# Optimization experiments

Measured on AMD Instinct MI355X. Metric: run time of the kernel, lower is better.

Reference implementation:

```python
import jax, jax.numpy as jnp
import numpy as np

B, L, D = 8, 4096, 1024
H, BS = 16, 4          # num_heads, block_size
d = D // H             # per-head dim


def setup_inputs() -> dict:
    ks = jax.random.split(jax.random.key(0), 4)
    x = jax.random.normal(ks[0], (B, L, D), dtype=jnp.float32)
    W_qkv = jax.random.normal(ks[1], (D, 3 * D), dtype=jnp.float32) * 0.02
    b_qkv = jnp.zeros((3 * D,), dtype=jnp.float32)
    W_proj = jax.random.normal(ks[2], (D, D), dtype=jnp.float32) * 0.02
    b_proj = jnp.zeros((D,), dtype=jnp.float32)
    return {"x": x, "W_qkv": W_qkv, "b_qkv": b_qkv,
            "W_proj": W_proj, "b_proj": b_proj}


def reference(x, W_qkv, b_qkv, W_proj, b_proj):
    scale = d ** -0.5
    n = L // BS  # number of blocks (L divisible by BS -> no padding/mask path)
    # qkv projection: (B, L, 3D); per-head layout [q(d) | k(d) | v(d)]
    qkv = x @ W_qkv + b_qkv
    qkv = qkv.reshape(B, L, H, 3 * d)
    q, k, v = qkv[..., :d], qkv[..., d:2 * d], qkv[..., 2 * d:]
    # (B, L, H, d) -> (B, H, n, BS, d)
    def to_blocks(t):
        return t.transpose(0, 2, 1, 3).reshape(B, H, n, BS, d)
    q, k, v = to_blocks(q), to_blocks(k), to_blocks(v)
    # block-local attention: tiny (BS x BS) score matrices per block
    attn = jnp.einsum('bhnid,bhnjd->bhnij', q, k) * scale
    attn = jax.nn.softmax(attn, axis=-1)
    o = jnp.einsum('bhnij,bhnjd->bhnid', attn, v)
    # (B, H, n, BS, d) -> (B, L, D)
    o = o.reshape(B, H, L, d).transpose(0, 2, 1, 3).reshape(B, L, D)
    return o @ W_proj + b_proj
```

## Files before the change

kernel.cpp:

```cpp
#include <hip/hip_runtime.h>
#include <hip/hip_bf16.h>

typedef __bf16 bf16_t;
typedef __bf16 bf16x4 __attribute__((ext_vector_type(4)));
typedef __bf16 bf16x8 __attribute__((ext_vector_type(8)));
typedef float  f32x4  __attribute__((ext_vector_type(4)));

#define D1   1024
#define D3   3072
#define NTOK 32768
#define NH   16

__device__ __forceinline__ void gl16(const void* g, void* l) {
  __builtin_amdgcn_global_load_lds(
      (__attribute__((address_space(1))) void*)(void*)g,
      (__attribute__((address_space(3))) void*)l, 16, 0, 0);
}

__global__ __launch_bounds__(256) void k0_convert(
    const float* __restrict__ x, bf16_t* __restrict__ xb)
{
  const size_t i = ((size_t)blockIdx.x * 256 + threadIdx.x) * 8;
  const float4 v0 = *reinterpret_cast<const float4*>(&x[i]);
  const float4 v1 = *reinterpret_cast<const float4*>(&x[i + 4]);
  bf16x8 o;
  o[0] = (bf16_t)v0.x; o[1] = (bf16_t)v0.y; o[2] = (bf16_t)v0.z; o[3] = (bf16_t)v0.w;
  o[4] = (bf16_t)v1.x; o[5] = (bf16_t)v1.y; o[6] = (bf16_t)v1.z; o[7] = (bf16_t)v1.w;
  *reinterpret_cast<bf16x8*>(&xb[i]) = o;
}

__global__ __launch_bounds__(256) void k0_transpose(
    const float* __restrict__ W, bf16_t* __restrict__ Wt, int K, int N)
{
  __shared__ float tile[32][33];
  const int k0 = blockIdx.x * 32, n0 = blockIdx.y * 32;
  const int tx = threadIdx.x & 31, ty = threadIdx.x >> 5;
#pragma unroll
  for (int i = 0; i < 4; ++i)
    tile[ty + i * 8][tx] = W[(size_t)(k0 + ty + i * 8) * N + n0 + tx];
  __syncthreads();
#pragma unroll
  for (int i = 0; i < 4; ++i)
    Wt[(size_t)(n0 + ty + i * 8) * K + k0 + tx] = (bf16_t)tile[tx][ty + i * 8];
}

__global__ __launch_bounds__(512, 4) void k1_qkv_attn(
    const bf16_t* __restrict__ xb, const bf16_t* __restrict__ Wt,
    const float* __restrict__ bqkv, bf16_t* __restrict__ o)
{
  __shared__ __align__(16) unsigned char smem[53248];
  bf16_t (*Ss)[200] = reinterpret_cast<bf16_t(*)[200]>(smem);
  float*  Ps        = reinterpret_cast<float*>(smem + 128 * 200 * 2);

  const int tid  = threadIdx.x;
  const int wv   = tid >> 6, lane = tid & 63;
  const int lrow = lane & 15, lkg = lane >> 4;
  const int wr   = wv >> 2, wc = wv & 3;
  const int m0   = blockIdx.x * 128;
  const int h    = blockIdx.y;

  const int lr = lane >> 3;
  const int lc = (lane & 7) * 8;
  const bf16_t* aS0 = xb + (size_t)(m0 + (wv * 2 + 0) * 8 + lr) * D1 + lc;
  const bf16_t* aS1 = xb + (size_t)(m0 + (wv * 2 + 1) * 8 + lr) * D1 + lc;
  char* aD0 = (char*)smem + (wv * 2 + 0) * 1024;
  char* aD1 = (char*)smem + (wv * 2 + 1) * 1024;
  const bf16_t* bS0 = Wt + (size_t)(h * 192 + (wv * 3 + 0) * 8 + lr) * D1 + lc;
  const bf16_t* bS1 = Wt + (size_t)(h * 192 + (wv * 3 + 1) * 8 + lr) * D1 + lc;
  const bf16_t* bS2 = Wt + (size_t)(h * 192 + (wv * 3 + 2) * 8 + lr) * D1 + lc;
  char* bD0 = (char*)smem + 16384 + (wv * 3 + 0) * 1024;
  char* bD1 = (char*)smem + 16384 + (wv * 3 + 1) * 1024;
  char* bD2 = (char*)smem + 16384 + (wv * 3 + 2) * 1024;

  f32x4 acc[4][3];
#pragma unroll
  for (int i = 0; i < 4; ++i)
#pragma unroll
    for (int j = 0; j < 3; ++j) {
      f32x4 z = {0.f, 0.f, 0.f, 0.f};
      acc[i][j] = z;
    }

  const char* As = (const char*)smem;
  const char* Bs = (const char*)smem + 16384;

  for (int k0 = 0; k0 < D1; k0 += 64) {
    gl16(aS0 + k0, aD0);
    gl16(aS1 + k0, aD1);
    gl16(bS0 + k0, bD0);
    gl16(bS1 + k0, bD1);
    gl16(bS2 + k0, bD2);
    __syncthreads();
#pragma unroll
    for (int kk = 0; kk < 2; ++kk) {
      bf16x8 a[4];
#pragma unroll
      for (int rf = 0; rf < 4; ++rf)
        a[rf] = *reinterpret_cast<const bf16x8*>(
            As + (wr * 64 + rf * 16 + lrow) * 128 + kk * 64 + lkg * 16);
#pragma unroll
      for (int cf = 0; cf < 3; ++cf) {
        const bf16x8 b = *reinterpret_cast<const bf16x8*>(
            Bs + (wc * 48 + cf * 16 + lrow) * 128 + kk * 64 + lkg * 16);
#pragma unroll
        for (int rf = 0; rf < 4; ++rf)
          acc[rf][cf] = __builtin_amdgcn_mfma_f32_16x16x32_bf16(
              a[rf], b, acc[rf][cf], 0, 0, 0);
      }
    }
    __syncthreads();
  }

#pragma unroll
  for (int cf = 0; cf < 3; ++cf) {
    const int col = wc * 48 + cf * 16 + lrow;
    const float bias = bqkv[h * 192 + col];
#pragma unroll
    for (int rf = 0; rf < 4; ++rf) {
      const int row = wr * 64 + rf * 16 + lkg * 4;
#pragma unroll
      for (int r = 0; r < 4; ++r)
        Ss[row + r][col] = (bf16_t)(acc[rf][cf][r] + bias);
    }
  }
  __syncthreads();

  {
    const int blk = tid >> 4, qi = (tid >> 2) & 3, kj = tid & 3;
    float s = 0.f;
#pragma unroll
    for (int c8 = 0; c8 < 8; ++c8) {
      const bf16x8 qv = *reinterpret_cast<const bf16x8*>(&Ss[blk * 4 + qi][c8 * 8]);
      const bf16x8 kv = *reinterpret_cast<const bf16x8*>(&Ss[blk * 4 + kj][64 + c8 * 8]);
#pragma unroll
      for (int u = 0; u < 8; ++u) s += (float)qv[u] * (float)kv[u];
    }
    s *= 0.125f;
    float mx = fmaxf(s, __shfl_xor(s, 1));
    mx = fmaxf(mx, __shfl_xor(mx, 2));
    const float e = __expf(s - mx);
    float sum = e + __shfl_xor(e, 1);
    sum += __shfl_xor(sum, 2);
    Ps[tid] = e / sum;
  }
  __syncthreads();

  {
    const int row = tid >> 2;
    const int blk = row >> 2, qi = row & 3;
    const int c0 = (tid & 3) * 16;
    const float p0 = Ps[blk * 16 + qi * 4 + 0];
    const float p1 = Ps[blk * 16 + qi * 4 + 1];
    const float p2 = Ps[blk * 16 + qi * 4 + 2];
    const float p3 = Ps[blk * 16 + qi * 4 + 3];
    bf16x8 outv[2];
#pragma unroll
    for (int hf = 0; hf < 2; ++hf) {
      const bf16x8 v0 = *reinterpret_cast<const bf16x8*>(&Ss[blk * 4 + 0][128 + c0 + hf * 8]);
      const bf16x8 v1 = *reinterpret_cast<const bf16x8*>(&Ss[blk * 4 + 1][128 + c0 + hf * 8]);
      const bf16x8 v2 = *reinterpret_cast<const bf16x8*>(&Ss[blk * 4 + 2][128 + c0 + hf * 8]);
      const bf16x8 v3 = *reinterpret_cast<const bf16x8*>(&Ss[blk * 4 + 3][128 + c0 + hf * 8]);
#pragma unroll
      for (int u = 0; u < 8; ++u)
        outv[hf][u] = (bf16_t)(p0 * (float)v0[u] + p1 * (float)v1[u] +
                               p2 * (float)v2[u] + p3 * (float)v3[u]);
    }
    bf16_t* dst = &o[(size_t)(m0 + row) * D1 + h * 64 + c0];
    *reinterpret_cast<bf16x8*>(dst)     = outv[0];
    *reinterpret_cast<bf16x8*>(dst + 8) = outv[1];
  }
}

__global__ __launch_bounds__(256, 2) void k2_proj(
    const bf16_t* __restrict__ o, const bf16_t* __restrict__ Wpt,
    const float* __restrict__ bp, float* __restrict__ out)
{
  __shared__ __align__(16) unsigned char smem2[32768];

  const int tid  = threadIdx.x;
  const int wv   = tid >> 6, lane = tid & 63;
  const int lrow = lane & 15, lkg = lane >> 4;
  const int wr   = wv >> 1, wc = wv & 1;
  const int m0   = blockIdx.x * 128, n0 = blockIdx.y * 128;

  const int lr = lane >> 3;
  const int lc = (lane & 7) * 8;
  const bf16_t* aSrc[4];
  const bf16_t* bSrc[4];
  char *aDst[4], *bDst[4];
#pragma unroll
  for (int i = 0; i < 4; ++i) {
    const int ch = wv * 4 + i;
    aSrc[i] = o   + (size_t)(m0 + ch * 8 + lr) * D1 + lc;
    bSrc[i] = Wpt + (size_t)(n0 + ch * 8 + lr) * D1 + lc;
    aDst[i] = (char*)smem2 + ch * 1024;
    bDst[i] = (char*)smem2 + 16384 + ch * 1024;
  }

  f32x4 acc[4][4];
#pragma unroll
  for (int i = 0; i < 4; ++i)
#pragma unroll
    for (int j = 0; j < 4; ++j) {
      f32x4 z = {0.f, 0.f, 0.f, 0.f};
      acc[i][j] = z;
    }

  const char* As = (const char*)smem2;
  const char* Bs = (const char*)smem2 + 16384;

  for (int k0 = 0; k0 < D1; k0 += 64) {
#pragma unroll
    for (int i = 0; i < 4; ++i) {
      gl16(aSrc[i] + k0, aDst[i]);
      gl16(bSrc[i] + k0, bDst[i]);
    }
    __syncthreads();
#pragma unroll
    for (int kk = 0; kk < 2; ++kk) {
      bf16x8 a[4], b[4];
#pragma unroll
      for (int rf = 0; rf < 4; ++rf)
        a[rf] = *reinterpret_cast<const bf16x8*>(
            As + (wr * 64 + rf * 16 + lrow) * 128 + kk * 64 + lkg * 16);
#pragma unroll
      for (int cf = 0; cf < 4; ++cf)
        b[cf] = *reinterpret_cast<const bf16x8*>(
            Bs + (wc * 64 + cf * 16 + lrow) * 128 + kk * 64 + lkg * 16);
#pragma unroll
      for (int rf = 0; rf < 4; ++rf)
#pragma unroll
        for (int cf = 0; cf < 4; ++cf)
          acc[rf][cf] = __builtin_amdgcn_mfma_f32_16x16x32_bf16(
              a[rf], b[cf], acc[rf][cf], 0, 0, 0);
    }
    __syncthreads();
  }

#pragma unroll
  for (int cf = 0; cf < 4; ++cf) {
    const int col = n0 + wc * 64 + cf * 16 + lrow;
    const float bias = bp[col];
#pragma unroll
    for (int rf = 0; rf < 4; ++rf) {
      const size_t row = (size_t)m0 + wr * 64 + rf * 16 + lkg * 4;
#pragma unroll
      for (int r = 0; r < 4; ++r)
        out[(row + r) * D1 + col] = acc[rf][cf][r] + bias;
    }
  }
}

extern "C" void kernel_launch(void* const* d_in, const int* in_sizes, int n_in,
                              void* d_out, int out_size, void* d_ws, size_t ws_size,
                              hipStream_t stream)
{
  const float* x    = (const float*)d_in[0];
  const float* Wqkv = (const float*)d_in[1];
  const float* bqkv = (const float*)d_in[2];
  const float* Wp   = (const float*)d_in[3];
  const float* bp   = (const float*)d_in[4];
  float* out        = (float*)d_out;

  bf16_t* xb   = (bf16_t*)d_ws;
  bf16_t* o_ws = xb   + (size_t)NTOK * D1;
  bf16_t* wtq  = o_ws + (size_t)NTOK * D1;
  bf16_t* wtp  = wtq  + (size_t)D3 * D1;

  k0_convert<<<NTOK * D1 / (256 * 8), 256, 0, stream>>>(x, xb);
  k0_transpose<<<dim3(D1 / 32, D3 / 32), 256, 0, stream>>>(Wqkv, wtq, D1, D3);
  k0_transpose<<<dim3(D1 / 32, D1 / 32), 256, 0, stream>>>(Wp,   wtp, D1, D1);
  k1_qkv_attn<<<dim3(NTOK / 128, NH), 512, 0, stream>>>(xb, wtq, bqkv, o_ws);
  k2_proj<<<dim3(NTOK / 128, D1 / 128), 256, 0, stream>>>(o_ws, wtp, bp, out);
}
```

Before: 603.8 us.

## Swizzle LDS layout, remap block order per XCD, raise occupancy bounds

Applies an XOR swizzle to the LDS tile layout in both GEMM kernels. Global-load source columns are permuted and the MFMA fragment reads use the matching XOR offset, which should remove LDS bank conflicts on the 128-byte-stride rows. Launches both kernels on a 1D grid and remaps block IDs so that blocks sharing an XCD (blockIdx mod 8) work on neighbouring tiles, improving L2 reuse of A rows and weights. Raises the launch_bounds min-blocks hint, which may force register spills.

```diff
diff --git a/kernel.cpp b/kernel.cpp
--- a/kernel.cpp
+++ b/kernel.cpp
@@ -2,7 +2,6 @@
 #include <hip/hip_bf16.h>
 
 typedef __bf16 bf16_t;
-typedef __bf16 bf16x4 __attribute__((ext_vector_type(4)));
 typedef __bf16 bf16x8 __attribute__((ext_vector_type(8)));
 typedef float  f32x4  __attribute__((ext_vector_type(4)));
 
@@ -44,7 +43,7 @@
     Wt[(size_t)(n0 + ty + i * 8) * K + k0 + tx] = (bf16_t)tile[tx][ty + i * 8];
 }
 
-__global__ __launch_bounds__(512, 4) void k1_qkv_attn(
+__global__ __launch_bounds__(512, 6) void k1_qkv_attn(
     const bf16_t* __restrict__ xb, const bf16_t* __restrict__ Wt,
     const float* __restrict__ bqkv, bf16_t* __restrict__ o)
 {
@@ -56,18 +55,20 @@
   const int wv   = tid >> 6, lane = tid & 63;
   const int lrow = lane & 15, lkg = lane >> 4;
   const int wr   = wv >> 2, wc = wv & 3;
-  const int m0   = blockIdx.x * 128;
-  const int h    = blockIdx.y;
-
-  const int lr = lane >> 3;
-  const int lc = (lane & 7) * 8;
-  const bf16_t* aS0 = xb + (size_t)(m0 + (wv * 2 + 0) * 8 + lr) * D1 + lc;
-  const bf16_t* aS1 = xb + (size_t)(m0 + (wv * 2 + 1) * 8 + lr) * D1 + lc;
+
+  const int logical = (blockIdx.x & 7) * 512 + (blockIdx.x >> 3);
+  const int h  = logical & 15;
+  const int m0 = (logical >> 4) * 128;
+
+  const int lr  = lane >> 3;
+  const int lcs = ((lane & 7) ^ lr) * 8;
+  const bf16_t* aS0 = xb + (size_t)(m0 + (wv * 2 + 0) * 8 + lr) * D1 + lcs;
+  const bf16_t* aS1 = xb + (size_t)(m0 + (wv * 2 + 1) * 8 + lr) * D1 + lcs;
   char* aD0 = (char*)smem + (wv * 2 + 0) * 1024;
   char* aD1 = (char*)smem + (wv * 2 + 1) * 1024;
-  const bf16_t* bS0 = Wt + (size_t)(h * 192 + (wv * 3 + 0) * 8 + lr) * D1 + lc;
-  const bf16_t* bS1 = Wt + (size_t)(h * 192 + (wv * 3 + 1) * 8 + lr) * D1 + lc;
-  const bf16_t* bS2 = Wt + (size_t)(h * 192 + (wv * 3 + 2) * 8 + lr) * D1 + lc;
+  const bf16_t* bS0 = Wt + (size_t)(h * 192 + (wv * 3 + 0) * 8 + lr) * D1 + lcs;
+  const bf16_t* bS1 = Wt + (size_t)(h * 192 + (wv * 3 + 1) * 8 + lr) * D1 + lcs;
+  const bf16_t* bS2 = Wt + (size_t)(h * 192 + (wv * 3 + 2) * 8 + lr) * D1 + lcs;
   char* bD0 = (char*)smem + 16384 + (wv * 3 + 0) * 1024;
   char* bD1 = (char*)smem + 16384 + (wv * 3 + 1) * 1024;
   char* bD2 = (char*)smem + 16384 + (wv * 3 + 2) * 1024;
@@ -83,6 +84,7 @@
 
   const char* As = (const char*)smem;
   const char* Bs = (const char*)smem + 16384;
+  const int sw = (lrow & 7) << 4;
 
   for (int k0 = 0; k0 < D1; k0 += 64) {
     gl16(aS0 + k0, aD0);
@@ -93,15 +95,16 @@
     __syncthreads();
 #pragma unroll
     for (int kk = 0; kk < 2; ++kk) {
+      const int koff = (kk * 64 + lkg * 16) ^ sw;
       bf16x8 a[4];
 #pragma unroll
       for (int rf = 0; rf < 4; ++rf)
         a[rf] = *reinterpret_cast<const bf16x8*>(
-            As + (wr * 64 + rf * 16 + lrow) * 128 + kk * 64 + lkg * 16);
+            As + (wr * 64 + rf * 16 + lrow) * 128 + koff);
 #pragma unroll
       for (int cf = 0; cf < 3; ++cf) {
         const bf16x8 b = *reinterpret_cast<const bf16x8*>(
-            Bs + (wc * 48 + cf * 16 + lrow) * 128 + kk * 64 + lkg * 16);
+            Bs + (wc * 48 + cf * 16 + lrow) * 128 + koff);
 #pragma unroll
         for (int rf = 0; rf < 4; ++rf)
           acc[rf][cf] = __builtin_amdgcn_mfma_f32_16x16x32_bf16(
@@ -171,7 +174,7 @@
   }
 }
 
-__global__ __launch_bounds__(256, 2) void k2_proj(
+__global__ __launch_bounds__(256, 3) void k2_proj(
     const bf16_t* __restrict__ o, const bf16_t* __restrict__ Wpt,
     const float* __restrict__ bp, float* __restrict__ out)
 {
@@ -181,18 +184,21 @@
   const int wv   = tid >> 6, lane = tid & 63;
   const int lrow = lane & 15, lkg = lane >> 4;
   const int wr   = wv >> 1, wc = wv & 1;
-  const int m0   = blockIdx.x * 128, n0 = blockIdx.y * 128;
-
-  const int lr = lane >> 3;
-  const int lc = (lane & 7) * 8;
+
+  const int logical = (blockIdx.x & 7) * 256 + (blockIdx.x >> 3);
+  const int n0 = (logical & 7) * 128;
+  const int m0 = (logical >> 3) * 128;
+
+  const int lr  = lane >> 3;
+  const int lcs = ((lane & 7) ^ lr) * 8;
   const bf16_t* aSrc[4];
   const bf16_t* bSrc[4];
   char *aDst[4], *bDst[4];
 #pragma unroll
   for (int i = 0; i < 4; ++i) {
     const int ch = wv * 4 + i;
-    aSrc[i] = o   + (size_t)(m0 + ch * 8 + lr) * D1 + lc;
-    bSrc[i] = Wpt + (size_t)(n0 + ch * 8 + lr) * D1 + lc;
+    aSrc[i] = o   + (size_t)(m0 + ch * 8 + lr) * D1 + lcs;
+    bSrc[i] = Wpt + (size_t)(n0 + ch * 8 + lr) * D1 + lcs;
     aDst[i] = (char*)smem2 + ch * 1024;
     bDst[i] = (char*)smem2 + 16384 + ch * 1024;
   }
@@ -208,6 +214,7 @@
 
   const char* As = (const char*)smem2;
   const char* Bs = (const char*)smem2 + 16384;
+  const int sw = (lrow & 7) << 4;
 
   for (int k0 = 0; k0 < D1; k0 += 64) {
 #pragma unroll
@@ -218,15 +225,16 @@
     __syncthreads();
 #pragma unroll
     for (int kk = 0; kk < 2; ++kk) {
+      const int koff = (kk * 64 + lkg * 16) ^ sw;
       bf16x8 a[4], b[4];
 #pragma unroll
       for (int rf = 0; rf < 4; ++rf)
         a[rf] = *reinterpret_cast<const bf16x8*>(
-            As + (wr * 64 + rf * 16 + lrow) * 128 + kk * 64 + lkg * 16);
+            As + (wr * 64 + rf * 16 + lrow) * 128 + koff);
 #pragma unroll
       for (int cf = 0; cf < 4; ++cf)
         b[cf] = *reinterpret_cast<const bf16x8*>(
-            Bs + (wc * 64 + cf * 16 + lrow) * 128 + kk * 64 + lkg * 16);
+            Bs + (wc * 64 + cf * 16 + lrow) * 128 + koff);
 #pragma unroll
       for (int rf = 0; rf < 4; ++rf)
 #pragma unroll
@@ -270,6 +278,6 @@
   k0_convert<<<NTOK * D1 / (256 * 8), 256, 0, stream>>>(x, xb);
   k0_transpose<<<dim3(D1 / 32, D3 / 32), 256, 0, stream>>>(Wqkv, wtq, D1, D3);
   k0_transpose<<<dim3(D1 / 32, D1 / 32), 256, 0, stream>>>(Wp,   wtp, D1, D1);
-  k1_qkv_attn<<<dim3(NTOK / 128, NH), 512, 0, stream>>>(xb, wtq, bqkv, o_ws);
-  k2_proj<<<dim3(NTOK / 128, D1 / 128), 256, 0, stream>>>(o_ws, wtp, bp, out);
-}
+  k1_qkv_attn<<<4096, 512, 0, stream>>>(xb, wtq, bqkv, o_ws);
+  k2_proj<<<2048, 256, 0, stream>>>(o_ws, wtp, bp, out);
+}
```

Result: slower. 881.1 us (+45.9%).
